# Performance work log

Measured on AMD Instinct MI355X. Metric: run time of the kernel, lower is better.

The kernel has to match this reference:

```python
import jax, jax.numpy as jnp
import numpy as np

NUM_HEADS = 16
NUM_KV_HEADS = 4
HEAD_DIM = 64
HIDDEN = 1024
B, S = 2, 2048


def setup_inputs() -> dict:
    key = jax.random.key(0)
    ks = jax.random.split(key, 9)
    sc = 0.02
    return {
        "x": jax.random.normal(ks[0], (B, S, HIDDEN), dtype=jnp.float32),
        "Wq": jax.random.normal(ks[1], (HIDDEN, NUM_HEADS * HEAD_DIM), dtype=jnp.float32) * sc,
        "bq": jnp.zeros((NUM_HEADS * HEAD_DIM,), dtype=jnp.float32),
        "Wk": jax.random.normal(ks[2], (HIDDEN, NUM_KV_HEADS * HEAD_DIM), dtype=jnp.float32) * sc,
        "bk": jnp.zeros((NUM_KV_HEADS * HEAD_DIM,), dtype=jnp.float32),
        "Wv": jax.random.normal(ks[3], (HIDDEN, NUM_KV_HEADS * HEAD_DIM), dtype=jnp.float32) * sc,
        "bv": jnp.zeros((NUM_KV_HEADS * HEAD_DIM,), dtype=jnp.float32),
        "Wo": jax.random.normal(ks[4], (NUM_HEADS * HEAD_DIM, HIDDEN), dtype=jnp.float32) * sc,
        "bo": jnp.zeros((HIDDEN,), dtype=jnp.float32),
    }


def reference(x, Wq, bq, Wk, bk, Wv, bv, Wo, bo):
    bs, seq, _ = x.shape
    groups = NUM_HEADS // NUM_KV_HEADS
    # projections -> [B, H, S, D]
    q = (x @ Wq + bq).reshape(bs, seq, NUM_HEADS, HEAD_DIM).transpose(0, 2, 1, 3)
    k = (x @ Wk + bk).reshape(bs, seq, NUM_KV_HEADS, HEAD_DIM).transpose(0, 2, 1, 3)
    v = (x @ Wv + bv).reshape(bs, seq, NUM_KV_HEADS, HEAD_DIM).transpose(0, 2, 1, 3)
    # repeat_interleave KV heads to match query heads (GQA expansion)
    k = jnp.repeat(k, groups, axis=1)
    v = jnp.repeat(v, groups, axis=1)
    # NOTE: source applies NO 1/sqrt(d) scaling and no mask/ALiBi
    scores = jnp.einsum("bhqd,bhkd->bhqk", q, k)
    attn = jax.nn.softmax(scores.astype(jnp.float32), axis=-1).astype(q.dtype)
    out = jnp.einsum("bhqk,bhkd->bhqd", attn, v)
    out = out.transpose(0, 2, 1, 3).reshape(bs, seq, NUM_HEADS * HEAD_DIM)
    return out @ Wo + bo
```

## Files before the change

kernel.cpp:

```cpp
#include <hip/hip_runtime.h>

#define NHEADS 16
#define NKV    4
#define HDIM   64
#define HIDDEN 1024
#define BATCH  2
#define SEQ    2048
#define MROWS  (BATCH * SEQ)
#define LOG2E  1.44269504088896340736f

typedef __bf16 bf16_t;
typedef bf16_t bf16x8 __attribute__((ext_vector_type(8)));
typedef float  f32x4  __attribute__((ext_vector_type(4)));

template<int N>  struct ic { static constexpr int  v = N; };
template<bool B> struct bc { static constexpr bool v = B; };

__device__ __forceinline__ float bf2f(unsigned short u) {
    return __uint_as_float(((unsigned int)u) << 16);
}
__device__ __forceinline__ unsigned short f2bf(float f) {
    unsigned int u = __float_as_uint(f);
    u += 0x7FFFu + ((u >> 16) & 1u);
    return (unsigned short)(u >> 16);
}

__device__ __forceinline__ void gld16(const unsigned short* g, unsigned short* l)
{
    __builtin_amdgcn_global_load_lds(
        (const __attribute__((address_space(1))) void*)g,
        (__attribute__((address_space(3))) void*)l,
        16, 0, 0);
}

__device__ __forceinline__ int swz(int row, int ch) {
    return (row * 8 + (ch ^ (row & 7))) * 8;
}

__device__ __forceinline__ bool sniff_is_f32(const unsigned short* __restrict__ x)
{
    const int e = (x[threadIdx.x & 63] >> 7) & 0xFF;
    const unsigned long long ok = __ballot(e >= 110 && e <= 140);
    return __popcll(ok) < 56;
}

__device__ __forceinline__ void load8cvt(const void* base, size_t elem, bool isf32, unsigned short out[8])
{
    if (!isf32) {
        *(uint4*)out = *(const uint4*)((const unsigned short*)base + elem);
    } else {
        const float* p = (const float*)base + elem;
        float4 v0 = *(const float4*)p;
        float4 v1 = *(const float4*)(p + 4);
        out[0] = f2bf(v0.x); out[1] = f2bf(v0.y); out[2] = f2bf(v0.z); out[3] = f2bf(v0.w);
        out[4] = f2bf(v1.x); out[5] = f2bf(v1.y); out[6] = f2bf(v1.z); out[7] = f2bf(v1.w);
    }
}
__device__ __forceinline__ float bias_at(const void* b, int i, bool isf32)
{
    return isf32 ? ((const float*)b)[i] : bf2f(((const unsigned short*)b)[i]);
}

__global__ __launch_bounds__(256)
void prep_kernel(const void* __restrict__ x,
                 const void* __restrict__ Wq, const void* __restrict__ Wk,
                 const void* __restrict__ Wv, const void* __restrict__ Wo,
                 unsigned short* __restrict__ xb,
                 unsigned short* __restrict__ Wqkvt,
                 unsigned short* __restrict__ Wot)
{
    const bool isf32 = sniff_is_f32((const unsigned short*)x);
    const int t = threadIdx.x;
    int bid = blockIdx.x;

    if (bid < 2048) {
        if (!isf32) return;
        const size_t c = (size_t)bid * 256 + t;
        unsigned short v[8];
        load8cvt(x, c * 8, true, v);
        *(uint4*)(&xb[c * 8]) = *(uint4*)v;
        return;
    }
    bid -= 2048;
    const void* src; unsigned short* dst; int N, rowoff;
    if (bid < 256)      {             src = Wq; dst = Wqkvt; N = 1024; rowoff = 0;    }
    else if (bid < 320) { bid -= 256; src = Wk; dst = Wqkvt; N = 256;  rowoff = 1024; }
    else if (bid < 384) { bid -= 320; src = Wv; dst = Wqkvt; N = 256;  rowoff = 1280; }
    else                { bid -= 384; src = Wo; dst = Wot;   N = 1024; rowoff = 0;    }
    const int ntx = N / 64;
    const int gn0 = (bid % ntx) * 64;
    const int gk0 = (bid / ntx) * 64;

    __shared__ unsigned short Ts[64][72];
#pragma unroll
    for (int half = 0; half < 2; ++half) {
        const int kl = (t >> 3) + half * 32;
        const int n8 = (t & 7) * 8;
        unsigned short v[8];
        load8cvt(src, (size_t)(gk0 + kl) * N + gn0 + n8, isf32, v);
        *(uint4*)(&Ts[kl][n8]) = *(uint4*)v;
    }
    __syncthreads();
#pragma unroll
    for (int half = 0; half < 2; ++half) {
        const int nl = (t >> 3) + half * 32;
        const int k8 = (t & 7) * 8;
        unsigned short v[8];
#pragma unroll
        for (int j = 0; j < 8; ++j) v[j] = Ts[k8 + j][nl];
        *(uint4*)(&dst[(size_t)(rowoff + gn0 + nl) * HIDDEN + gk0 + k8]) = *(uint4*)v;
    }
}

template<int KK>
__device__ __forceinline__ void gemm_tile(const unsigned short* __restrict__ A,
                                          const unsigned short* __restrict__ Bt,
                                          int m0, int n0,
                                          unsigned short* As, unsigned short* Bs,
                                          f32x4 (&acc)[2][2])
{
    static_assert(KK / 64 == 16, "pipeline schedule assumes 16 K-steps");
    const int tid  = threadIdx.x;
    const int lane = tid & 63;
    const int wave = tid >> 6;
    const int quad = lane >> 4;
    const int l15  = lane & 15;
    const int wr   = wave >> 1;
    const int wc   = wave & 1;

    const int srow = tid >> 3;
    const int gch  = ((tid & 7) ^ (srow & 7)) * 8;

    const unsigned short* ga[2];
    const unsigned short* gb[2];
#pragma unroll
    for (int r = 0; r < 2; ++r) {
        ga[r] = A  + (size_t)(m0 + srow + r * 32) * KK + gch;
        gb[r] = Bt + (size_t)(n0 + srow + r * 32) * KK + gch;
    }
    unsigned short* const adst = As + wave * 512;
    unsigned short* const bdst = Bs + wave * 512;

    int aoffs[2][2], boffs[2][2];
#pragma unroll
    for (int kk = 0; kk < 2; ++kk) {
#pragma unroll
        for (int i = 0; i < 2; ++i) {
            aoffs[kk][i] = swz(wr * 32 + i * 16 + l15, kk * 4 + quad);
            boffs[kk][i] = swz(wc * 32 + i * 16 + l15, kk * 4 + quad);
        }
    }

#define GSTAGE(B)                                                \
    do {                                                         \
        gld16(ga[0], adst + (B) * 4096);        ga[0] += 64;     \
        gld16(ga[1], adst + (B) * 4096 + 2048); ga[1] += 64;     \
        gld16(gb[0], bdst + (B) * 4096);        gb[0] += 64;     \
        gld16(gb[1], bdst + (B) * 4096 + 2048); gb[1] += 64;     \
    } while (0)

    GSTAGE(0);
    GSTAGE(1);

    auto step = [&](auto B_, auto STG_, auto LAST_) {
        constexpr int B = decltype(B_)::v;
        if constexpr (decltype(LAST_)::v) asm volatile("s_waitcnt vmcnt(0)" ::: "memory");
        else                              asm volatile("s_waitcnt vmcnt(4)" ::: "memory");
        __builtin_amdgcn_sched_barrier(0);
        __builtin_amdgcn_s_barrier();
        __builtin_amdgcn_sched_barrier(0);
        if constexpr (decltype(STG_)::v) GSTAGE((B + 2) % 3);

#pragma unroll
        for (int kk = 0; kk < 2; ++kk) {
            bf16x8 af[2], bfv[2];
#pragma unroll
            for (int i = 0; i < 2; ++i) {
                af[i]  = *(const bf16x8*)(&As[B * 4096 + aoffs[kk][i]]);
                bfv[i] = *(const bf16x8*)(&Bs[B * 4096 + boffs[kk][i]]);
            }
            __builtin_amdgcn_s_setprio(1);
#pragma unroll
            for (int i = 0; i < 2; ++i)
#pragma unroll
                for (int j = 0; j < 2; ++j)
                    acc[i][j] = __builtin_amdgcn_mfma_f32_16x16x32_bf16(af[i], bfv[j], acc[i][j], 0, 0, 0);
            __builtin_amdgcn_s_setprio(0);
        }
    };

#pragma unroll 1
    for (int k0 = 0; k0 < 12; k0 += 3) {
        step(ic<0>{}, bc<true>{}, bc<false>{});
        step(ic<1>{}, bc<true>{}, bc<false>{});
        step(ic<2>{}, bc<true>{}, bc<false>{});
    }
    step(ic<0>{}, bc<true>{},  bc<false>{});
    step(ic<1>{}, bc<true>{},  bc<false>{});
    step(ic<2>{}, bc<false>{}, bc<false>{});
    step(ic<0>{}, bc<false>{}, bc<true>{});
#undef GSTAGE
}

__global__ __launch_bounds__(256)
void gemm_qkv(const void* __restrict__ xraw,
              const unsigned short* __restrict__ xb,
              const unsigned short* __restrict__ Bt,
              const void* __restrict__ bq, const void* __restrict__ bk,
              const void* __restrict__ bv,
              unsigned short* __restrict__ Qh,
              unsigned short* __restrict__ Kh,
              unsigned short* __restrict__ Vt)
{
    __shared__ __align__(16) unsigned short As[3 * 64 * 64];
    __shared__ __align__(16) unsigned short Bs[3 * 64 * 64];
    const bool bias_f32 = sniff_is_f32((const unsigned short*)xraw);
    const unsigned short* A = bias_f32 ? xb : (const unsigned short*)xraw;
    const int lane = threadIdx.x & 63;
    const int wave = threadIdx.x >> 6;
    const int quad = lane >> 4, l15 = lane & 15;
    const int wr = wave >> 1, wc = wave & 1;
    const int m0 = blockIdx.y * 64, n0 = blockIdx.x * 64;

    f32x4 acc[2][2] = {};
    gemm_tile<HIDDEN>(A, Bt, m0, n0, As, Bs, acc);

#pragma unroll
    for (int i = 0; i < 2; ++i) {
#pragma unroll
        for (int j = 0; j < 2; ++j) {
            const int nn  = n0 + wc * 32 + j * 16 + l15;
            const int mmb = m0 + wr * 32 + i * 16 + quad * 4;
            const int b = mmb >> 11, s0 = mmb & 2047;
            if (nn < 1024) {
                const float bias = bias_at(bq, nn, bias_f32);
                const int h = nn >> 6, d = nn & 63;
                const size_t idx0 = (((size_t)(b * NHEADS + h)) * SEQ + s0) * 64 + d;
#pragma unroll
                for (int r = 0; r < 4; ++r)
                    Qh[idx0 + (size_t)r * 64] = f2bf((acc[i][j][r] + bias) * LOG2E);
            } else if (nn < 1280) {
                const int nk = nn - 1024;
                const float bias = bias_at(bk, nk, bias_f32);
                const int h = nk >> 6, d = nk & 63;
                const size_t idx0 = (((size_t)(b * NKV + h)) * SEQ + s0) * 64 + d;
#pragma unroll
                for (int r = 0; r < 4; ++r)
                    Kh[idx0 + (size_t)r * 64] = f2bf(acc[i][j][r] + bias);
            } else {
                const int nv = nn - 1280;
                const float bias = bias_at(bv, nv, bias_f32);
                const int h = nv >> 6, d = nv & 63;
                const size_t idx = (((size_t)(b * NKV + h)) * 64 + d) * SEQ + s0;
                unsigned short vv[4];
#pragma unroll
                for (int r = 0; r < 4; ++r) vv[r] = f2bf(acc[i][j][r] + bias);
                *(uint2*)(&Vt[idx]) = *(uint2*)vv;
            }
        }
    }
}

__global__ __launch_bounds__(256)
void gemm_o(const void* __restrict__ xraw,
            const unsigned short* __restrict__ A,
            const unsigned short* __restrict__ Bt,
            const void* __restrict__ bo,
            float* __restrict__ out)
{
    __shared__ __align__(16) unsigned short As[3 * 64 * 64];
    __shared__ __align__(16) unsigned short Bs[3 * 64 * 64];
    const bool bias_f32 = sniff_is_f32((const unsigned short*)xraw);
    const int lane = threadIdx.x & 63;
    const int wave = threadIdx.x >> 6;
    const int quad = lane >> 4, l15 = lane & 15;
    const int wr = wave >> 1, wc = wave & 1;
    const int m0 = blockIdx.y * 64, n0 = blockIdx.x * 64;

    f32x4 acc[2][2] = {};
    gemm_tile<HIDDEN>(A, Bt, m0, n0, As, Bs, acc);

#pragma unroll
    for (int i = 0; i < 2; ++i) {
#pragma unroll
        for (int j = 0; j < 2; ++j) {
            const int nn = n0 + wc * 32 + j * 16 + l15;
            const float bvv = bias_at(bo, nn, bias_f32);
#pragma unroll
            for (int r = 0; r < 4; ++r) {
                const int mm = m0 + wr * 32 + i * 16 + quad * 4 + r;
                out[(size_t)mm * HIDDEN + nn] = acc[i][j][r] + bvv;
            }
        }
    }
}

#define NT    (SEQ / 64)
#define KVOFF (64 * 64)

__global__ __launch_bounds__(256)
void attn_kernel(const unsigned short* __restrict__ Qh,
                 const unsigned short* __restrict__ Kh,
                 const unsigned short* __restrict__ Vt,
                 unsigned short* __restrict__ O)
{
    __shared__ __align__(16) unsigned short Kth[3 * KVOFF];
    __shared__ __align__(16) unsigned short VtT[3 * KVOFF];
    __shared__ __align__(16) unsigned short Pt[4 * 32 * 64];

    const int tid  = threadIdx.x;
    const int lane = tid & 63;
    const int wave = tid >> 6;
    const int quad = lane >> 4;
    const int l15  = lane & 15;

    const int qt = blockIdx.x;
    const int h  = blockIdx.y;
    const int b  = blockIdx.z;
    const int kv = h >> 2;

    const size_t qoff = ((size_t)(b * NHEADS + h)) * SEQ * HDIM;
    const size_t koff = ((size_t)(b * NKV + kv)) * SEQ * HDIM;
    const size_t voff = ((size_t)(b * NKV + kv)) * HDIM * SEQ;

    const int q0 = qt * 128 + wave * 32;

    bf16x8 qf0[2], qf1[2];
#pragma unroll
    for (int qs = 0; qs < 2; ++qs) {
        const size_t qrow = qoff + (size_t)(q0 + qs * 16 + l15) * HDIM;
        qf0[qs] = *(const bf16x8*)(&Qh[qrow + quad * 8]);
        qf1[qs] = *(const bf16x8*)(&Qh[qrow + 32 + quad * 8]);
    }

    bf16x8 onesv;
#pragma unroll
    for (int i = 0; i < 8; ++i) onesv[i] = (bf16_t)1.0f;

    f32x4 o0[4] = {}, o1[4] = {};
    f32x4 lacc0 = {}, lacc1 = {};

    int koff0[4], koff1[4], pwoff[2][4], proff[2], voffs[2][4];
#pragma unroll
    for (int j = 0; j < 4; ++j) {
        koff0[j] = swz(j * 16 + l15, quad);
        koff1[j] = swz(j * 16 + l15, quad ^ 4);
#pragma unroll
        for (int qs = 0; qs < 2; ++qs)
            pwoff[qs][j] = wave * 2048 + swz(qs * 16 + l15, j * 2 + (quad >> 1)) + (quad & 1) * 4;
    }
#pragma unroll
    for (int kk = 0; kk < 2; ++kk) {
        proff[kk] = wave * 2048 + swz(l15, kk * 4 + quad);
#pragma unroll
        for (int dt = 0; dt < 4; ++dt)
            voffs[kk][dt] = swz(dt * 16 + l15, kk * 4 + quad);
    }

    const unsigned short* kp = Kh + koff;
    const unsigned short* vp = Vt + voff;
    const int srow0 = tid >> 3;
    const int gch_s = ((tid & 7) ^ (srow0 & 7)) * 8;
    unsigned short* const kdst = Kth + wave * 512;
    unsigned short* const vdst = VtT + wave * 512;

#define ATTN_STAGE(B)                                                            \
    do {                                                                         \
        gld16(kp + (size_t)srow0 * HDIM + gch_s,        kdst + (B) * KVOFF);        \
        gld16(kp + (size_t)(srow0 + 32) * HDIM + gch_s, kdst + (B) * KVOFF + 2048); \
        gld16(vp + (size_t)srow0 * SEQ + gch_s,         vdst + (B) * KVOFF);        \
        gld16(vp + (size_t)(srow0 + 32) * SEQ + gch_s,  vdst + (B) * KVOFF + 2048); \
        kp += 64 * HDIM; vp += 64;                                               \
    } while (0)

    ATTN_STAGE(0);
    ATTN_STAGE(1);

    auto step = [&](auto B_, auto STG_, auto LAST_) {
        constexpr int B = decltype(B_)::v;
        if constexpr (decltype(LAST_)::v) asm volatile("s_waitcnt vmcnt(0)" ::: "memory");
        else                              asm volatile("s_waitcnt vmcnt(4)" ::: "memory");
        __builtin_amdgcn_sched_barrier(0);
        __builtin_amdgcn_s_barrier();
        __builtin_amdgcn_sched_barrier(0);
        if constexpr (decltype(STG_)::v) ATTN_STAGE((B + 2) % 3);

#pragma unroll
        for (int j = 0; j < 4; ++j) {
            const bf16x8 kh0 = *(const bf16x8*)(&Kth[B * KVOFF + koff0[j]]);
            const bf16x8 kh1 = *(const bf16x8*)(&Kth[B * KVOFF + koff1[j]]);
#pragma unroll
            for (int qs = 0; qs < 2; ++qs) {
                f32x4 z = {};
                __builtin_amdgcn_s_setprio(1);
                z = __builtin_amdgcn_mfma_f32_16x16x32_bf16(kh0, qs ? qf0[1] : qf0[0], z, 0, 0, 0);
                const f32x4 sc = __builtin_amdgcn_mfma_f32_16x16x32_bf16(kh1, qs ? qf1[1] : qf1[0], z, 0, 0, 0);
                __builtin_amdgcn_s_setprio(0);
                const float p0 = __builtin_amdgcn_exp2f(sc[0]);
                const float p1 = __builtin_amdgcn_exp2f(sc[1]);
                const float p2 = __builtin_amdgcn_exp2f(sc[2]);
                const float p3 = __builtin_amdgcn_exp2f(sc[3]);
                uint2 w;
                w.x = __builtin_amdgcn_perm(__float_as_uint(p1), __float_as_uint(p0), 0x07060302u);
                w.y = __builtin_amdgcn_perm(__float_as_uint(p3), __float_as_uint(p2), 0x07060302u);
                *(uint2*)(&Pt[pwoff[qs][j]]) = w;
            }
        }

#pragma unroll
        for (int kk = 0; kk < 2; ++kk) {
            const bf16x8 pf0 = *(const bf16x8*)(&Pt[proff[kk]]);
            const bf16x8 pf1 = *(const bf16x8*)(&Pt[proff[kk] + 1024]);
            __builtin_amdgcn_s_setprio(1);
            lacc0 = __builtin_amdgcn_mfma_f32_16x16x32_bf16(onesv, pf0, lacc0, 0, 0, 0);
            lacc1 = __builtin_amdgcn_mfma_f32_16x16x32_bf16(onesv, pf1, lacc1, 0, 0, 0);
#pragma unroll
            for (int dt = 0; dt < 4; ++dt) {
                const bf16x8 vf = *(const bf16x8*)(&VtT[B * KVOFF + voffs[kk][dt]]);
                o0[dt] = __builtin_amdgcn_mfma_f32_16x16x32_bf16(vf, pf0, o0[dt], 0, 0, 0);
                o1[dt] = __builtin_amdgcn_mfma_f32_16x16x32_bf16(vf, pf1, o1[dt], 0, 0, 0);
            }
            __builtin_amdgcn_s_setprio(0);
        }
    };

#pragma unroll 1
    for (int t0 = 0; t0 < 30; t0 += 3) {
        step(ic<0>{}, bc<true>{}, bc<false>{});
        step(ic<1>{}, bc<true>{}, bc<false>{});
        step(ic<2>{}, bc<true>{}, bc<false>{});
    }
    step(ic<0>{}, bc<false>{}, bc<false>{});
    step(ic<1>{}, bc<false>{}, bc<true>{});
#undef ATTN_STAGE

#pragma unroll
    for (int qs = 0; qs < 2; ++qs) {
        const float inv = 1.0f / (qs ? lacc1[0] : lacc0[0]);
        const size_t rowbase = ((size_t)b * SEQ + (q0 + qs * 16 + l15)) * (NHEADS * HDIM) + h * HDIM;
#pragma unroll
        for (int dt = 0; dt < 4; ++dt) {
            const f32x4 ov = qs ? o1[dt] : o0[dt];
            unsigned short v4[4];
#pragma unroll
            for (int r = 0; r < 4; ++r) v4[r] = f2bf(ov[r] * inv);
            *(uint2*)(&O[rowbase + dt * 16 + quad * 4]) = *(uint2*)v4;
        }
    }
}

extern "C" void kernel_launch(void* const* d_in, const int* in_sizes, int n_in,
                              void* d_out, int out_size, void* d_ws, size_t ws_size,
                              hipStream_t stream)
{
    const void* x  = d_in[0];
    const void* Wq = d_in[1];
    const void* bq = d_in[2];
    const void* Wk = d_in[3];
    const void* bk = d_in[4];
    const void* Wv = d_in[5];
    const void* bv = d_in[6];
    const void* Wo = d_in[7];
    const void* bo = d_in[8];
    float* out = (float*)d_out;

    unsigned short* p = (unsigned short*)d_ws;
    unsigned short* xb    = p; p += (size_t)MROWS * HIDDEN;
    unsigned short* Wqkvt = p; p += (size_t)1536 * HIDDEN;
    unsigned short* Wot   = p; p += (size_t)HIDDEN * HIDDEN;
    unsigned short* Qh = p;  p += (size_t)MROWS * 1024;
    unsigned short* Kh = p;  p += (size_t)2 * NKV * SEQ * HDIM;
    unsigned short* Vt = p;  p += (size_t)2 * NKV * SEQ * HDIM;
    unsigned short* A2 = p;  p += (size_t)MROWS * 1024;

    dim3 blk(256);
    prep_kernel<<<dim3(2688), blk, 0, stream>>>(x, Wq, Wk, Wv, Wo, xb, Wqkvt, Wot);
    gemm_qkv<<<dim3(1536 / 64, MROWS / 64), blk, 0, stream>>>(
        x, xb, Wqkvt, bq, bk, bv, Qh, Kh, Vt);
    attn_kernel<<<dim3(SEQ / 128, NHEADS, BATCH), blk, 0, stream>>>(Qh, Kh, Vt, A2);
    gemm_o<<<dim3(1024 / 64, MROWS / 64), blk, 0, stream>>>(x, A2, Wot, bo, out);
}
```

Before: 182.1 us.

## Enlarge GEMM tiles to 128x128 with double-buffered K pipeline

The QKV and output projection GEMMs move from 64x64 block tiles to 128x128, with each wave computing a 64x64 sub-tile (4x4 MFMA fragments). The hand-scheduled three-stage pipeline with explicit vmcnt waits is replaced by a simpler two-buffer loop using __syncthreads. This aims to raise data reuse per global load and MFMA density per wave. In exchange it cuts the block count sharply (256 blocks for the output GEMM), which may underfill the GPU and expose more load latency because the deeper prefetch is gone.

```diff
diff --git a/kernel.cpp b/kernel.cpp
--- a/kernel.cpp
+++ b/kernel.cpp
@@ -117,9 +117,8 @@
                                           const unsigned short* __restrict__ Bt,
                                           int m0, int n0,
                                           unsigned short* As, unsigned short* Bs,
-                                          f32x4 (&acc)[2][2])
-{
-    static_assert(KK / 64 == 16, "pipeline schedule assumes 16 K-steps");
+                                          f32x4 (&acc)[4][4])
+{
     const int tid  = threadIdx.x;
     const int lane = tid & 63;
     const int wave = tid >> 6;
@@ -131,74 +130,60 @@
     const int srow = tid >> 3;
     const int gch  = ((tid & 7) ^ (srow & 7)) * 8;
 
-    const unsigned short* ga[2];
-    const unsigned short* gb[2];
-#pragma unroll
-    for (int r = 0; r < 2; ++r) {
-        ga[r] = A  + (size_t)(m0 + srow + r * 32) * KK + gch;
-        gb[r] = Bt + (size_t)(n0 + srow + r * 32) * KK + gch;
+    const unsigned short* ga[4];
+    const unsigned short* gb[4];
+#pragma unroll
+    for (int r = 0; r < 4; ++r) {
+        ga[r] = A  + (size_t)(m0 + r * 32 + srow) * KK + gch;
+        gb[r] = Bt + (size_t)(n0 + r * 32 + srow) * KK + gch;
     }
     unsigned short* const adst = As + wave * 512;
     unsigned short* const bdst = Bs + wave * 512;
 
-    int aoffs[2][2], boffs[2][2];
+    int aoffs[2][4], boffs[2][4];
 #pragma unroll
     for (int kk = 0; kk < 2; ++kk) {
 #pragma unroll
-        for (int i = 0; i < 2; ++i) {
-            aoffs[kk][i] = swz(wr * 32 + i * 16 + l15, kk * 4 + quad);
-            boffs[kk][i] = swz(wc * 32 + i * 16 + l15, kk * 4 + quad);
-        }
-    }
-
-#define GSTAGE(B)                                                \
-    do {                                                         \
-        gld16(ga[0], adst + (B) * 4096);        ga[0] += 64;     \
-        gld16(ga[1], adst + (B) * 4096 + 2048); ga[1] += 64;     \
-        gld16(gb[0], bdst + (B) * 4096);        gb[0] += 64;     \
-        gld16(gb[1], bdst + (B) * 4096 + 2048); gb[1] += 64;     \
+        for (int i = 0; i < 4; ++i) {
+            aoffs[kk][i] = swz(wr * 64 + i * 16 + l15, kk * 4 + quad);
+            boffs[kk][i] = swz(wc * 64 + i * 16 + l15, kk * 4 + quad);
+        }
+    }
+
+#define GSTAGE(B)                                                     \
+    do {                                                              \
+        _Pragma("unroll")                                             \
+        for (int r = 0; r < 4; ++r) {                                 \
+            gld16(ga[r], adst + (B) * 8192 + r * 2048); ga[r] += 64;  \
+            gld16(gb[r], bdst + (B) * 8192 + r * 2048); gb[r] += 64;  \
+        }                                                             \
     } while (0)
 
+    constexpr int nk = KK / 64;
     GSTAGE(0);
-    GSTAGE(1);
-
-    auto step = [&](auto B_, auto STG_, auto LAST_) {
-        constexpr int B = decltype(B_)::v;
-        if constexpr (decltype(LAST_)::v) asm volatile("s_waitcnt vmcnt(0)" ::: "memory");
-        else                              asm volatile("s_waitcnt vmcnt(4)" ::: "memory");
-        __builtin_amdgcn_sched_barrier(0);
-        __builtin_amdgcn_s_barrier();
-        __builtin_amdgcn_sched_barrier(0);
-        if constexpr (decltype(STG_)::v) GSTAGE((B + 2) % 3);
+#pragma unroll 2
+    for (int k = 0; k < nk; ++k) {
+        const int cur = k & 1;
+        __syncthreads();
+        if (k + 1 < nk) GSTAGE(cur ^ 1);
 
 #pragma unroll
         for (int kk = 0; kk < 2; ++kk) {
-            bf16x8 af[2], bfv[2];
-#pragma unroll
-            for (int i = 0; i < 2; ++i) {
-                af[i]  = *(const bf16x8*)(&As[B * 4096 + aoffs[kk][i]]);
-                bfv[i] = *(const bf16x8*)(&Bs[B * 4096 + boffs[kk][i]]);
+            bf16x8 af[4], bfv[4];
+#pragma unroll
+            for (int i = 0; i < 4; ++i) {
+                af[i]  = *(const bf16x8*)(&As[cur * 8192 + aoffs[kk][i]]);
+                bfv[i] = *(const bf16x8*)(&Bs[cur * 8192 + boffs[kk][i]]);
             }
             __builtin_amdgcn_s_setprio(1);
 #pragma unroll
-            for (int i = 0; i < 2; ++i)
-#pragma unroll
-                for (int j = 0; j < 2; ++j)
+            for (int i = 0; i < 4; ++i)
+#pragma unroll
+                for (int j = 0; j < 4; ++j)
                     acc[i][j] = __builtin_amdgcn_mfma_f32_16x16x32_bf16(af[i], bfv[j], acc[i][j], 0, 0, 0);
             __builtin_amdgcn_s_setprio(0);
         }
-    };
-
-#pragma unroll 1
-    for (int k0 = 0; k0 < 12; k0 += 3) {
-        step(ic<0>{}, bc<true>{}, bc<false>{});
-        step(ic<1>{}, bc<true>{}, bc<false>{});
-        step(ic<2>{}, bc<true>{}, bc<false>{});
-    }
-    step(ic<0>{}, bc<true>{},  bc<false>{});
-    step(ic<1>{}, bc<true>{},  bc<false>{});
-    step(ic<2>{}, bc<false>{}, bc<false>{});
-    step(ic<0>{}, bc<false>{}, bc<true>{});
+    }
 #undef GSTAGE
 }
 
@@ -212,25 +197,25 @@
               unsigned short* __restrict__ Kh,
               unsigned short* __restrict__ Vt)
 {
-    __shared__ __align__(16) unsigned short As[3 * 64 * 64];
-    __shared__ __align__(16) unsigned short Bs[3 * 64 * 64];
+    __shared__ __align__(16) unsigned short As[2 * 128 * 64];
+    __shared__ __align__(16) unsigned short Bs[2 * 128 * 64];
     const bool bias_f32 = sniff_is_f32((const unsigned short*)xraw);
     const unsigned short* A = bias_f32 ? xb : (const unsigned short*)xraw;
     const int lane = threadIdx.x & 63;
     const int wave = threadIdx.x >> 6;
     const int quad = lane >> 4, l15 = lane & 15;
     const int wr = wave >> 1, wc = wave & 1;
-    const int m0 = blockIdx.y * 64, n0 = blockIdx.x * 64;
-
-    f32x4 acc[2][2] = {};
+    const int m0 = blockIdx.y * 128, n0 = blockIdx.x * 128;
+
+    f32x4 acc[4][4] = {};
     gemm_tile<HIDDEN>(A, Bt, m0, n0, As, Bs, acc);
 
 #pragma unroll
-    for (int i = 0; i < 2; ++i) {
-#pragma unroll
-        for (int j = 0; j < 2; ++j) {
-            const int nn  = n0 + wc * 32 + j * 16 + l15;
-            const int mmb = m0 + wr * 32 + i * 16 + quad * 4;
+    for (int i = 0; i < 4; ++i) {
+#pragma unroll
+        for (int j = 0; j < 4; ++j) {
+            const int nn  = n0 + wc * 64 + j * 16 + l15;
+            const int mmb = m0 + wr * 64 + i * 16 + quad * 4;
             const int b = mmb >> 11, s0 = mmb & 2047;
             if (nn < 1024) {
                 const float bias = bias_at(bq, nn, bias_f32);
@@ -268,27 +253,27 @@
             const void* __restrict__ bo,
             float* __restrict__ out)
 {
-    __shared__ __align__(16) unsigned short As[3 * 64 * 64];
-    __shared__ __align__(16) unsigned short Bs[3 * 64 * 64];
+    __shared__ __align__(16) unsigned short As[2 * 128 * 64];
+    __shared__ __align__(16) unsigned short Bs[2 * 128 * 64];
     const bool bias_f32 = sniff_is_f32((const unsigned short*)xraw);
     const int lane = threadIdx.x & 63;
     const int wave = threadIdx.x >> 6;
     const int quad = lane >> 4, l15 = lane & 15;
     const int wr = wave >> 1, wc = wave & 1;
-    const int m0 = blockIdx.y * 64, n0 = blockIdx.x * 64;
-
-    f32x4 acc[2][2] = {};
+    const int m0 = blockIdx.y * 128, n0 = blockIdx.x * 128;
+
+    f32x4 acc[4][4] = {};
     gemm_tile<HIDDEN>(A, Bt, m0, n0, As, Bs, acc);
 
 #pragma unroll
-    for (int i = 0; i < 2; ++i) {
-#pragma unroll
-        for (int j = 0; j < 2; ++j) {
-            const int nn = n0 + wc * 32 + j * 16 + l15;
+    for (int i = 0; i < 4; ++i) {
+#pragma unroll
+        for (int j = 0; j < 4; ++j) {
+            const int nn = n0 + wc * 64 + j * 16 + l15;
             const float bvv = bias_at(bo, nn, bias_f32);
 #pragma unroll
             for (int r = 0; r < 4; ++r) {
-                const int mm = m0 + wr * 32 + i * 16 + quad * 4 + r;
+                const int mm = m0 + wr * 64 + i * 16 + quad * 4 + r;
                 out[(size_t)mm * HIDDEN + nn] = acc[i][j][r] + bvv;
             }
         }
@@ -475,8 +460,8 @@
 
     dim3 blk(256);
     prep_kernel<<<dim3(2688), blk, 0, stream>>>(x, Wq, Wk, Wv, Wo, xb, Wqkvt, Wot);
-    gemm_qkv<<<dim3(1536 / 64, MROWS / 64), blk, 0, stream>>>(
+    gemm_qkv<<<dim3(1536 / 128, MROWS / 128), blk, 0, stream>>>(
         x, xb, Wqkvt, bq, bk, bv, Qh, Kh, Vt);
     attn_kernel<<<dim3(SEQ / 128, NHEADS, BATCH), blk, 0, stream>>>(Qh, Kh, Vt, A2);
-    gemm_o<<<dim3(1024 / 64, MROWS / 64), blk, 0, stream>>>(x, A2, Wot, bo, out);
-}
+    gemm_o<<<dim3(1024 / 128, MROWS / 128), blk, 0, stream>>>(x, A2, Wot, bo, out);
+}
```

Measured after the change: 179.8 us. About the same (-1.2%).
